# Optimization experiments

Hardware: AMD Instinct MI355X
Metric: run time of the kernel (lower is better)

Reference implementation:

```python
import jax, jax.numpy as jnp
import numpy as np

DIM = 2048
N_HEADS = 16
N_KV_HEADS = 8
HEAD_DIM = DIM // N_HEADS  # 128
N_REP = N_HEADS // N_KV_HEADS
BATCH = 2
SEQ = 2048
CHUNK = 128  # chunked-parallel causal linear attention; SEQ % CHUNK == 0


def _make_freqs_cis(seq_len, head_dim, theta=10000.0):
    freqs = 1.0 / (theta ** (np.arange(0, head_dim, 2, dtype=np.float32) / head_dim))
    t = np.arange(seq_len, dtype=np.float32)
    ang = np.outer(t, freqs)  # [S, D/2]
    return jnp.asarray(np.stack([np.cos(ang), np.sin(ang)], axis=-1))  # [S, D/2, 2]


def setup_inputs() -> dict:
    key = jax.random.key(0)
    ks = jax.random.split(key, 5)
    x = jax.random.normal(ks[0], (BATCH, SEQ, DIM), dtype=jnp.float32)
    freqs_cis = _make_freqs_cis(SEQ, HEAD_DIM)
    s = 0.02
    wq = s * jax.random.normal(ks[1], (N_HEADS * HEAD_DIM, DIM), dtype=jnp.float32)
    wk = s * jax.random.normal(ks[2], (N_KV_HEADS * HEAD_DIM, DIM), dtype=jnp.float32)
    wv = s * jax.random.normal(ks[3], (N_KV_HEADS * HEAD_DIM, DIM), dtype=jnp.float32)
    wo = s * jax.random.normal(ks[4], (DIM, N_HEADS * HEAD_DIM), dtype=jnp.float32)
    return {"x": x, "freqs_cis": freqs_cis, "wq": wq, "wk": wk, "wv": wv, "wo": wo}


def _apply_rotary(x, freqs_cis):
    # x: [B, S, H, D]; freqs_cis: [S, D/2, 2] (cos, sin). Llama pairing: (x0,x1),(x2,x3),...
    B, S, H, D = x.shape
    xr = x.reshape(B, S, H, D // 2, 2)
    x0, x1 = xr[..., 0], xr[..., 1]
    c = freqs_cis[None, :, None, :, 0]
    s = freqs_cis[None, :, None, :, 1]
    o0 = x0 * c - x1 * s
    o1 = x0 * s + x1 * c
    return jnp.stack([o0, o1], axis=-1).reshape(B, S, H, D)


def _causal_linear_attention(q, k, v):
    # q, k, v: [B, H, S, D]; output_i = q_i @ sum_{j<=i} k_j^T v_j
    B, H, S, D = q.shape
    q = jax.nn.softmax(q * (D ** -0.5), axis=-1)  # softmax over feature dim
    k = jax.nn.softmax(k, axis=2)                 # softmax over sequence dim (as in source)
    Nc = S // CHUNK
    qc = q.reshape(B, H, Nc, CHUNK, D)
    kc = k.reshape(B, H, Nc, CHUNK, D)
    vc = v.reshape(B, H, Nc, CHUNK, D)
    # per-chunk KV outer-product sums: [B, H, Nc, D, D]
    kv = jnp.einsum('bhncd,bhnce->bhnde', kc, vc)
    cum = jnp.cumsum(kv, axis=2)
    cum_excl = jnp.concatenate([jnp.zeros_like(cum[:, :, :1]), cum[:, :, :-1]], axis=2)
    inter = jnp.einsum('bhncd,bhnde->bhnce', qc, cum_excl)
    scores = jnp.einsum('bhncd,bhnmd->bhncm', qc, kc)  # [B,H,Nc,C,C]
    mask = jnp.tril(jnp.ones((CHUNK, CHUNK), dtype=bool))
    scores = jnp.where(mask, scores, jnp.zeros((), dtype=scores.dtype))
    intra = jnp.einsum('bhncm,bhnme->bhnce', scores, vc)
    return (inter + intra).reshape(B, H, S, D)


def reference(x, freqs_cis, wq, wk, wv, wo):
    B, S, _ = x.shape
    xq = (x @ wq.T).reshape(B, S, N_HEADS, HEAD_DIM)
    xk = (x @ wk.T).reshape(B, S, N_KV_HEADS, HEAD_DIM)
    xv = (x @ wv.T).reshape(B, S, N_KV_HEADS, HEAD_DIM)
    xq = _apply_rotary(xq, freqs_cis)
    xk = _apply_rotary(xk, freqs_cis)
    # repeat_kv: each kv head repeated N_REP consecutive times
    keys = jnp.repeat(xk, N_REP, axis=2)
    values = jnp.repeat(xv, N_REP, axis=2)
    q = jnp.transpose(xq, (0, 2, 1, 3))
    k = jnp.transpose(keys, (0, 2, 1, 3))
    v = jnp.transpose(values, (0, 2, 1, 3))
    out = _causal_linear_attention(q, k, v)  # [B, H, S, D]
    out = jnp.transpose(out, (0, 2, 1, 3)).reshape(B, S, N_HEADS * HEAD_DIM)
    return out @ wo.T
```

## Files before the change

kernel.cpp:

```cpp
#include <hip/hip_runtime.h>
#include <math.h>

#define DIMV 2048
#define NHEAD 16
#define NKV 8
#define HD 128
#define BATCH 2
#define SEQ 2048
#define CHUNK 128
#define NCHUNK 16
#define MTOK 4096
#define KVD (NKV * HD)

typedef _Float16 half8_t __attribute__((ext_vector_type(8)));
typedef _Float16 half4_t __attribute__((ext_vector_type(4)));
typedef _Float16 half2_t __attribute__((ext_vector_type(2)));
typedef float f32x4 __attribute__((ext_vector_type(4)));

#define GLOBAL_AS __attribute__((address_space(1)))
#define LDS_AS __attribute__((address_space(3)))

#define BARX() __builtin_amdgcn_s_barrier()
#define WAITL(n) asm volatile("s_waitcnt lgkmcnt(" #n ")" ::: "memory")
#define WAITVM(n) asm volatile("s_waitcnt vmcnt(" #n ")" ::: "memory")

__global__ __launch_bounds__(256) void cast_all(const float* __restrict__ x,
                                                const float* __restrict__ wq,
                                                const float* __restrict__ wk,
                                                const float* __restrict__ wv,
                                                const float* __restrict__ wo,
                                                _Float16* __restrict__ xh,
                                                _Float16* __restrict__ wqkvh,
                                                _Float16* __restrict__ woh,
                                                const float* __restrict__ fc,
                                                float* __restrict__ fcT) {
  __shared__ float T[64][65];
  if (blockIdx.x >= 10240) {
    int q = blockIdx.x - 10240;
    int s0 = (q & 31) * 64, d0 = (q >> 5) * 64;
    int t = threadIdx.x;
    int r = t >> 4, c4 = (t & 15) * 4;
#pragma unroll
    for (int p = 0; p < 4; ++p) {
      int sr = p * 16 + r;
      float4 v = *(const float4*)&fc[(size_t)(s0 + sr) * 128 + d0 + c4];
      T[sr][c4] = v.x; T[sr][c4 + 1] = v.y; T[sr][c4 + 2] = v.z; T[sr][c4 + 3] = v.w;
    }
    __syncthreads();
#pragma unroll
    for (int p = 0; p < 4; ++p) {
      int dr = p * 16 + r;
      float4 v = make_float4(T[c4][dr], T[c4 + 1][dr], T[c4 + 2][dr], T[c4 + 3][dr]);
      *(float4*)&fcT[(size_t)(d0 + dr) * SEQ + s0 + c4] = v;
    }
    return;
  }
  long i = (long)(blockIdx.x * 256 + threadIdx.x) * 8;
  const float* src;
  _Float16* dst;
  long off;
  if (i < 8388608)        { src = x;  dst = xh;              off = 0; }
  else if (i < 12582912)  { src = wq; dst = wqkvh;           off = 8388608; }
  else if (i < 14680064)  { src = wk; dst = wqkvh + 4194304; off = 12582912; }
  else if (i < 16777216)  { src = wv; dst = wqkvh + 6291456; off = 14680064; }
  else                    { src = wo; dst = woh;             off = 16777216; }
  long e = i - off;
  float4 a = *(const float4*)&src[e];
  float4 b = *(const float4*)&src[e + 4];
  half8_t h = {(_Float16)a.x, (_Float16)a.y, (_Float16)a.z, (_Float16)a.w,
               (_Float16)b.x, (_Float16)b.y, (_Float16)b.z, (_Float16)b.w};
  *(half8_t*)&dst[e] = h;
}

#define STG_A(bb, kk, i, k0)                                                      \
  __builtin_amdgcn_global_load_lds(                                               \
      (const GLOBAL_AS void*)(A + aoff + (size_t)(i) * 128 * 2048 + (k0) + (kk) * 32), \
      (LDS_AS void*)(As + ((bb) * 2 + (kk)) * 8192 + (i) * 4096 + wave * 512), 16, 0, 0)
#define STG_B(bb, kk, i, k0)                                                      \
  __builtin_amdgcn_global_load_lds(                                               \
      (const GLOBAL_AS void*)(B + boff + (size_t)(i) * 128 * 2048 + (k0) + (kk) * 32), \
      (LDS_AS void*)(Bs + ((bb) * 2 + (kk)) * 8192 + (i) * 4096 + wave * 512), 16, 0, 0)

#define LDA_F(bb, kk, ih) do {                                                    \
    const _Float16* pA_ = As + ((bb) * 2 + (kk)) * 8192 +                         \
                          (wr * 128 + (ih) * 64 + m16) * 32 + pseg8;              \
    af[0] = *(const half8_t*)(pA_);                                               \
    af[1] = *(const half8_t*)(pA_ + 512);                                         \
    af[2] = *(const half8_t*)(pA_ + 1024);                                        \
    af[3] = *(const half8_t*)(pA_ + 1536);                                        \
  } while (0)
#define LDB_F(bb, kk) do {                                                        \
    const _Float16* pB_ = Bs + ((bb) * 2 + (kk)) * 8192 +                         \
                          (wc * 64 + m16) * 32 + pseg8;                           \
    bf[0] = *(const half8_t*)(pB_);                                               \
    bf[1] = *(const half8_t*)(pB_ + 512);                                         \
    bf[2] = *(const half8_t*)(pB_ + 1024);                                        \
    bf[3] = *(const half8_t*)(pB_ + 1536);                                        \
  } while (0)

#define MMX(ih) do {                                                              \
    _Pragma("unroll")                                                             \
    for (int i_ = 0; i_ < 4; ++i_)                                                \
      _Pragma("unroll")                                                           \
      for (int j_ = 0; j_ < 4; ++j_)                                              \
        acc[(ih) * 4 + i_][j_] = __builtin_amdgcn_mfma_f32_16x16x32_f16(          \
            af[i_], bf[j_], acc[(ih) * 4 + i_][j_], 0, 0, 0);                     \
  } while (0)

#define KTILE(bb, k0, DS1, DS2, DS3, DS4, VA, VB) do {                            \
  half8_t af[4], bf[4];                                                           \
  LDA_F(bb, 0, 0); LDB_F(bb, 0);                                                  \
  if (DS1) { STG_A(1 - (bb), 1, 0, (k0) + 64); STG_A(1 - (bb), 1, 1, (k0) + 64); } \
  BARX(); WAITL(0);                                                               \
  __builtin_amdgcn_s_setprio(1); MMX(0); __builtin_amdgcn_s_setprio(0);           \
  BARX();                                                                         \
  LDA_F(bb, 0, 1);                                                                \
  if (DS2) { STG_B(1 - (bb), 1, 0, (k0) + 64); STG_B(1 - (bb), 1, 1, (k0) + 64); } \
  WAITVM(VA);                                                                     \
  BARX(); WAITL(0);                                                               \
  __builtin_amdgcn_s_setprio(1); MMX(1); __builtin_amdgcn_s_setprio(0);           \
  BARX();                                                                         \
  LDA_F(bb, 1, 0); LDB_F(bb, 1);                                                  \
  if (DS3) { STG_A(bb, 0, 0, (k0) + 128); STG_A(bb, 0, 1, (k0) + 128); }          \
  BARX(); WAITL(0);                                                               \
  __builtin_amdgcn_s_setprio(1); MMX(0); __builtin_amdgcn_s_setprio(0);           \
  BARX();                                                                         \
  LDA_F(bb, 1, 1);                                                                \
  if (DS4) { STG_B(bb, 0, 0, (k0) + 128); STG_B(bb, 0, 1, (k0) + 128); }          \
  WAITVM(VB);                                                                     \
  BARX(); WAITL(0);                                                               \
  __builtin_amdgcn_s_setprio(1); MMX(1); __builtin_amdgcn_s_setprio(0);           \
  BARX();                                                                         \
} while (0)

__global__ __launch_bounds__(512, 2) void hgemm_qkv_8p(const _Float16* __restrict__ A,
                                                       const _Float16* __restrict__ B,
                                                       const float* __restrict__ fc,
                                                       _Float16* __restrict__ qh,
                                                       _Float16* __restrict__ kT,
                                                       _Float16* __restrict__ vT) {
  const int K = 2048;
  __shared__ _Float16 As[32768];
  __shared__ _Float16 Bs[32768];
  __shared__ float qsum[4][256];

  const int tid = threadIdx.x;
  const int lane = tid & 63;
  const int wave = tid >> 6;
  const int wr = wave >> 2;
  const int wc = wave & 3;
  const int m16 = lane & 15, quad = lane >> 4;
  const int row0 = blockIdx.y * 256, col0 = blockIdx.x * 256;
  const int pseg8 = (quad ^ ((m16 >> 1) & 3)) * 8;

  const int r_ld = tid >> 2;
  const int sseg = (tid & 3) ^ ((tid >> 3) & 3);
  const size_t aoff = (size_t)(row0 + r_ld) * K + sseg * 8;
  const size_t boff = (size_t)(col0 + r_ld) * K + sseg * 8;

  f32x4 acc[8][4];
#pragma unroll
  for (int m = 0; m < 8; ++m)
#pragma unroll
    for (int j = 0; j < 4; ++j) acc[m][j] = (f32x4){0.f, 0.f, 0.f, 0.f};

  STG_A(0, 0, 0, 0); STG_A(0, 0, 1, 0); STG_B(0, 0, 0, 0); STG_B(0, 0, 1, 0);
  STG_A(0, 1, 0, 0); STG_A(0, 1, 1, 0); STG_B(0, 1, 0, 0); STG_B(0, 1, 1, 0);
  STG_A(1, 0, 0, 64); STG_A(1, 0, 1, 64); STG_B(1, 0, 0, 64); STG_B(1, 0, 1, 64);
  WAITVM(8);
  BARX();

  for (int t = 0; t < 30; t += 2) {
    KTILE(0, t * 64,      1, 1, 1, 1, 8, 8);
    KTILE(1, t * 64 + 64, 1, 1, 1, 1, 8, 8);
  }
  KTILE(0, 1920, 1, 1, 0, 0, 8, 4);
  KTILE(1, 1984, 0, 0, 0, 0, 0, 0);

  if (col0 < 2048) {
    const float sc = 0.08838834764831845f;
    float psum[8][4];
#pragma unroll
    for (int m = 0; m < 8; ++m)
#pragma unroll
      for (int r = 0; r < 4; ++r) psum[m][r] = 0.f;
#pragma unroll
    for (int m = 0; m < 8; ++m)
#pragma unroll
      for (int j = 0; j < 4; ++j) {
        int dl2 = (wc * 64 + j * 16 + m16) & 126;
#pragma unroll
        for (int r = 0; r < 4; ++r) {
          float val = acc[m][j][r];
          float par = __shfl_xor(val, 1);
          int row_l = wr * 128 + (m >> 2) * 64 + (m & 3) * 16 + quad * 4 + r;
          int s_tok = (row0 + row_l) & (SEQ - 1);
          float2 cs = *(const float2*)&fc[(size_t)s_tok * 128 + dl2];
          float o = val * cs.x + par * ((m16 & 1) ? cs.y : -cs.y);
          float e = __expf(o * sc);
          acc[m][j][r] = e;
          psum[m][r] += e;
        }
      }
#pragma unroll
    for (int mm = 1; mm < 16; mm <<= 1)
#pragma unroll
      for (int m = 0; m < 8; ++m)
#pragma unroll
        for (int r = 0; r < 4; ++r) psum[m][r] += __shfl_xor(psum[m][r], mm);
    if (m16 == 0) {
#pragma unroll
      for (int m = 0; m < 8; ++m)
#pragma unroll
        for (int r = 0; r < 4; ++r) {
          int row_l = wr * 128 + (m >> 2) * 64 + (m & 3) * 16 + quad * 4 + r;
          qsum[wc][row_l] = psum[m][r];
        }
    }
    __syncthreads();
#pragma unroll
    for (int m = 0; m < 8; ++m)
#pragma unroll
      for (int r = 0; r < 4; ++r) {
        int row_l = wr * 128 + (m >> 2) * 64 + (m & 3) * 16 + quad * 4 + r;
        psum[m][r] = 1.f / (qsum[wc & 2][row_l] + qsum[(wc & 2) | 1][row_l]);
      }
#pragma unroll
    for (int m = 0; m < 8; ++m)
#pragma unroll
      for (int j = 0; j < 4; ++j) {
        int col = col0 + wc * 64 + j * 16 + m16;
#pragma unroll
        for (int r = 0; r < 4; ++r) {
          int row_l = wr * 128 + (m >> 2) * 64 + (m & 3) * 16 + quad * 4 + r;
          qh[(size_t)(row0 + row_l) * DIMV + col] = (_Float16)(acc[m][j][r] * psum[m][r]);
        }
      }
  } else {
#pragma unroll
    for (int m = 0; m < 8; ++m)
#pragma unroll
      for (int j = 0; j < 4; ++j) {
        int col = col0 + wc * 64 + j * 16 + m16;
        int rowb = row0 + wr * 128 + (m >> 2) * 64 + (m & 3) * 16 + quad * 4;
        half4_t hv = {(_Float16)acc[m][j][0], (_Float16)acc[m][j][1],
                      (_Float16)acc[m][j][2], (_Float16)acc[m][j][3]};
        if (col0 < 3072) {
          *(half4_t*)&kT[(size_t)(col - 2048) * MTOK + rowb] = hv;
        } else {
          *(half4_t*)&vT[(size_t)(col - 3072) * MTOK + rowb] = hv;
        }
      }
  }
}

#define STGBT(bb, kk, k0) do {                                                    \
  __builtin_amdgcn_global_load_lds(                                               \
      (const GLOBAL_AS void*)(A + abase + (k0) + (kk) * 32),                      \
      (LDS_AS void*)(As + ((bb) * 2 + (kk)) * 4096 + wave * 512), 16, 0, 0);      \
  __builtin_amdgcn_global_load_lds(                                               \
      (const GLOBAL_AS void*)(B + bbase + (k0) + (kk) * 32),                      \
      (LDS_AS void*)(Bs + ((bb) * 2 + (kk)) * 8192 + wave * 512), 16, 0, 0);      \
  __builtin_amdgcn_global_load_lds(                                               \
      (const GLOBAL_AS void*)(B + bbase + (size_t)128 * 2048 + (k0) + (kk) * 32), \
      (LDS_AS void*)(Bs + ((bb) * 2 + (kk)) * 8192 + 4096 + wave * 512), 16, 0, 0);\
} while (0)

#define PHASE_BT(bb, kk, SEN, sbb, skk, sk0, VM) do {                             \
  WAITVM(VM);                                                                     \
  BARX();                                                                         \
  half8_t af[4], bf[4];                                                           \
  const _Float16* pA_ = As + ((bb) * 2 + (kk)) * 4096 +                           \
                        (wr * 64 + m16) * 32 + pseg8;                             \
  const _Float16* pB_ = Bs + ((bb) * 2 + (kk)) * 8192 +                           \
                        (wc * 64 + m16) * 32 + pseg8;                             \
  af[0] = *(const half8_t*)(pA_);        af[1] = *(const half8_t*)(pA_ + 512);    \
  af[2] = *(const half8_t*)(pA_ + 1024); af[3] = *(const half8_t*)(pA_ + 1536);   \
  bf[0] = *(const half8_t*)(pB_);        bf[1] = *(const half8_t*)(pB_ + 512);    \
  bf[2] = *(const half8_t*)(pB_ + 1024); bf[3] = *(const half8_t*)(pB_ + 1536);   \
  if (SEN) STGBT(sbb, skk, sk0);                                                  \
  WAITL(0);                                                                       \
  __builtin_amdgcn_s_setprio(1);                                                  \
  _Pragma("unroll")                                                               \
  for (int i_ = 0; i_ < 4; ++i_)                                                  \
    _Pragma("unroll")                                                             \
    for (int j_ = 0; j_ < 4; ++j_)                                                \
      acc[i_][j_] = __builtin_amdgcn_mfma_f32_16x16x32_f16(                       \
          af[i_], bf[j_], acc[i_][j_], 0, 0, 0);                                  \
  __builtin_amdgcn_s_setprio(0);                                                  \
} while (0)

__global__ __launch_bounds__(512, 2) void hgemm_bt_8p(const _Float16* __restrict__ A,
                                                      const _Float16* __restrict__ B,
                                                      float* __restrict__ C) {
  const int K = 2048, N = 2048;
  __shared__ _Float16 As[16384];
  __shared__ _Float16 Bs[32768];

  const int tid = threadIdx.x;
  const int lane = tid & 63;
  const int wave = tid >> 6;
  const int wr = wave >> 2;
  const int wc = wave & 3;
  const int m16 = lane & 15, quad = lane >> 4;
  const int row0 = blockIdx.y * 128, col0 = blockIdx.x * 256;
  const int pseg8 = (quad ^ ((m16 >> 1) & 3)) * 8;

  const int r_ld = tid >> 2;
  const int sseg = (tid & 3) ^ ((tid >> 3) & 3);
  const size_t abase = (size_t)(row0 + r_ld) * K + sseg * 8;
  const size_t bbase = (size_t)(col0 + r_ld) * K + sseg * 8;

  f32x4 acc[4][4];
#pragma unroll
  for (int i = 0; i < 4; ++i)
#pragma unroll
    for (int j = 0; j < 4; ++j) acc[i][j] = (f32x4){0.f, 0.f, 0.f, 0.f};

  STGBT(0, 0, 0); STGBT(0, 1, 0); STGBT(1, 0, 64);

  for (int t = 0; t < 30; ++t) {
    const int bb = t & 1;
    const int k0 = t * 64;
    PHASE_BT(bb, 0, 1, bb ^ 1, 1, k0 + 64, 6);
    PHASE_BT(bb, 1, 1, bb, 0, k0 + 128, 6);
  }
  PHASE_BT(0, 0, 1, 1, 1, 1984, 6);
  PHASE_BT(0, 1, 0, 0, 0, 0, 6);
  PHASE_BT(1, 0, 0, 0, 0, 0, 3);
  PHASE_BT(1, 1, 0, 0, 0, 0, 0);

#pragma unroll
  for (int i = 0; i < 4; ++i)
#pragma unroll
    for (int j = 0; j < 4; ++j) {
      int col = col0 + wc * 64 + j * 16 + m16;
      int rowb = row0 + wr * 64 + i * 16 + quad * 4;
#pragma unroll
      for (int r = 0; r < 4; ++r) C[(size_t)(rowb + r) * N + col] = acc[i][j][r];
    }
}

__global__ __launch_bounds__(256) void k_rope_softmax_T(_Float16* __restrict__ kT,
                                                        const float* __restrict__ fcT) {
  int bi = blockIdx.x;
  int b = bi & 1, pr = bi >> 1;
  int d0 = pr * 2, dl = d0 & 127;
  int t = threadIdx.x;
  size_t r0 = (size_t)d0 * MTOK + b * SEQ + t * 8;
  size_t r1 = r0 + MTOK;
  half8_t x0v = *(half8_t*)&kT[r0];
  half8_t x1v = *(half8_t*)&kT[r1];
  int s8 = t * 8;
  float4 ca = *(const float4*)&fcT[(size_t)dl * SEQ + s8];
  float4 cb = *(const float4*)&fcT[(size_t)dl * SEQ + s8 + 4];
  float4 sa = *(const float4*)&fcT[(size_t)(dl + 1) * SEQ + s8];
  float4 sb = *(const float4*)&fcT[(size_t)(dl + 1) * SEQ + s8 + 4];
  float cc[8] = {ca.x, ca.y, ca.z, ca.w, cb.x, cb.y, cb.z, cb.w};
  float ss[8] = {sa.x, sa.y, sa.z, sa.w, sb.x, sb.y, sb.z, sb.w};
  float e0[8], e1[8];
  float sum0 = 0.f, sum1 = 0.f;
#pragma unroll
  for (int j = 0; j < 8; ++j) {
    float x0 = (float)x0v[j], x1 = (float)x1v[j];
    float o0 = x0 * cc[j] - x1 * ss[j];
    float o1 = x0 * ss[j] + x1 * cc[j];
    e0[j] = expf(o0); e1[j] = expf(o1);
    sum0 += e0[j]; sum1 += e1[j];
  }
#pragma unroll
  for (int off = 1; off < 64; off <<= 1) {
    sum0 += __shfl_xor(sum0, off);
    sum1 += __shfl_xor(sum1, off);
  }
  __shared__ float red[8];
  if ((t & 63) == 0) { red[(t >> 6) * 2] = sum0; red[(t >> 6) * 2 + 1] = sum1; }
  __syncthreads();
  float S0 = red[0] + red[2] + red[4] + red[6];
  float S1 = red[1] + red[3] + red[5] + red[7];
  float i0 = 1.f / S0, i1 = 1.f / S1;
  half8_t w0, w1;
#pragma unroll
  for (int j = 0; j < 8; ++j) {
    w0[j] = (_Float16)(e0[j] * i0);
    w1[j] = (_Float16)(e1[j] * i1);
  }
  *(half8_t*)&kT[r0] = w0;
  *(half8_t*)&kT[r1] = w1;
}

__global__ __launch_bounds__(256) void transpose_k(const _Float16* __restrict__ kT,
                                                   _Float16* __restrict__ kh) {
  __shared__ _Float16 T[64][65];
  int t0 = blockIdx.x * 64, d0 = blockIdx.y * 64;
  int t = threadIdx.x;
  int r = t >> 3, c8 = (t & 7) * 8;
#pragma unroll
  for (int p = 0; p < 2; ++p) {
    int dr = p * 32 + r;
    half8_t v = *(const half8_t*)&kT[(size_t)(d0 + dr) * MTOK + t0 + c8];
#pragma unroll
    for (int j = 0; j < 8; ++j) T[c8 + j][dr] = v[j];
  }
  __syncthreads();
#pragma unroll
  for (int p = 0; p < 2; ++p) {
    int tr = p * 32 + r;
    half8_t v;
#pragma unroll
    for (int j = 0; j < 8; ++j) v[j] = T[tr][c8 + j];
    *(half8_t*)&kh[(size_t)(t0 + tr) * KVD + d0 + c8] = v;
  }
}

__global__ __launch_bounds__(256) void kv_chunk_mfma(const _Float16* __restrict__ vT,
                                                     const _Float16* __restrict__ kT,
                                                     float* __restrict__ kvT) {
  __shared__ _Float16 As[2][128 * 32];
  __shared__ _Float16 Bs[2][128 * 32];
  int bi = blockIdx.x;
  int n = bi & 15, kvh = (bi >> 4) & 7, b = bi >> 7;
  int tok0 = b * SEQ + n * CHUNK;
  const int tid = threadIdx.x;
  const int lane = tid & 63;
  const int wave = tid >> 6;
  const int wr = wave & 1, wc = wave >> 1;
  const int m16 = lane & 15, quad = lane >> 4;
  const int qsw8 = (quad ^ ((m16 >> 1) & 3)) * 8;

  f32x4 acc[4][4];
#pragma unroll
  for (int i = 0; i < 4; ++i)
#pragma unroll
    for (int j = 0; j < 4; ++j) acc[i][j] = (f32x4){0.f, 0.f, 0.f, 0.f};

  const int r_ld = tid >> 2;
  const int sseg = (tid & 3) ^ ((tid >> 3) & 3);
  const size_t a_base = (size_t)(kvh * HD + r_ld) * MTOK + tok0 + sseg * 8;

#pragma unroll
  for (int i = 0; i < 2; ++i) {
    __builtin_amdgcn_global_load_lds(
        (const GLOBAL_AS void*)(vT + a_base + (size_t)i * 64 * MTOK),
        (LDS_AS void*)(&As[0][0] + i * 2048 + wave * 512), 16, 0, 0);
    __builtin_amdgcn_global_load_lds(
        (const GLOBAL_AS void*)(kT + a_base + (size_t)i * 64 * MTOK),
        (LDS_AS void*)(&Bs[0][0] + i * 2048 + wave * 512), 16, 0, 0);
  }

#pragma unroll
  for (int s = 0; s < 4; ++s) {
    WAITVM(0);
    BARX();
    if (s < 3) {
      const int k0 = (s + 1) * 32;
      const int bb = (s + 1) & 1;
#pragma unroll
      for (int i = 0; i < 2; ++i) {
        __builtin_amdgcn_global_load_lds(
            (const GLOBAL_AS void*)(vT + a_base + (size_t)i * 64 * MTOK + k0),
            (LDS_AS void*)(&As[bb][0] + i * 2048 + wave * 512), 16, 0, 0);
        __builtin_amdgcn_global_load_lds(
            (const GLOBAL_AS void*)(kT + a_base + (size_t)i * 64 * MTOK + k0),
            (LDS_AS void*)(&Bs[bb][0] + i * 2048 + wave * 512), 16, 0, 0);
      }
    }
    const _Float16* ra = &As[s & 1][0];
    const _Float16* rb = &Bs[s & 1][0];
    half8_t af[4], bf[4];
#pragma unroll
    for (int i = 0; i < 4; ++i) {
      af[i] = *(const half8_t*)&ra[(wr * 64 + i * 16 + m16) * 32 + qsw8];
      bf[i] = *(const half8_t*)&rb[(wc * 64 + i * 16 + m16) * 32 + qsw8];
    }
#pragma unroll
    for (int i = 0; i < 4; ++i)
#pragma unroll
      for (int j = 0; j < 4; ++j)
        acc[i][j] = __builtin_amdgcn_mfma_f32_16x16x32_f16(af[i], bf[j], acc[i][j], 0, 0, 0);
  }
#pragma unroll
  for (int i = 0; i < 4; ++i)
#pragma unroll
    for (int j = 0; j < 4; ++j) {
      int col = wc * 64 + j * 16 + m16;
      int rowb = wr * 64 + i * 16 + quad * 4;
#pragma unroll
      for (int r = 0; r < 4; ++r)
        kvT[(size_t)bi * 16384 + (size_t)(rowb + r) * 128 + col] = acc[i][j][r];
    }
}

__global__ __launch_bounds__(256) void cumsum_h(const float* __restrict__ kvT,
                                                _Float16* __restrict__ cumh) {
  int gid = blockIdx.x * 256 + threadIdx.x;
  int bk = gid >> 14, idx = gid & 16383;
  size_t base = (size_t)bk * NCHUNK * 16384 + idx;
  float run = 0.f;
#pragma unroll
  for (int n = 0; n < NCHUNK; ++n) {
    cumh[base + (size_t)n * 16384] = (_Float16)run;
    run += kvT[base + (size_t)n * 16384];
  }
}

__global__ __launch_bounds__(256) void attn_fused(const _Float16* __restrict__ qh,
                                                  const _Float16* __restrict__ kh,
                                                  const _Float16* __restrict__ cumh,
                                                  const _Float16* __restrict__ vT,
                                                  _Float16* __restrict__ ath) {
  __shared__ _Float16 QS[128 * 128];
  __shared__ _Float16 Bk[2][128 * 32];
  __shared__ _Float16 Bc[2][128 * 32];
  int bi = blockIdx.x;
  int n = bi & 15, h = (bi >> 4) & 15, b = bi >> 8;
  int kvh = h >> 1;
  int tok0 = b * SEQ + n * CHUNK;
  const int tid = threadIdx.x;
  const int lane = tid & 63;
  const int wave = tid >> 6;
  const int wr = wave & 1, wc = wave >> 1;
  const int m16 = lane & 15, quad = lane >> 4;
  const int qsw8 = (quad ^ ((m16 >> 1) & 3)) * 8;
  const int r_ld = tid >> 2;
  const int sseg = (tid & 3) ^ ((tid >> 3) & 3);

  f32x4 acc[4][4];
  f32x4 accs[4][4];
#pragma unroll
  for (int i = 0; i < 4; ++i)
#pragma unroll
    for (int j = 0; j < 4; ++j) {
      acc[i][j] = (f32x4){0.f, 0.f, 0.f, 0.f};
      accs[i][j] = (f32x4){0.f, 0.f, 0.f, 0.f};
    }

  const int qrow = tid >> 4;
  const int qsl = (tid & 15) ^ (qrow & 7);
  const size_t qsrc = (size_t)(tok0 + qrow) * DIMV + h * HD + qsl * 8;
#pragma unroll
  for (int p = 0; p < 8; ++p)
    __builtin_amdgcn_global_load_lds(
        (const GLOBAL_AS void*)(qh + qsrc + (size_t)p * 16 * DIMV),
        (LDS_AS void*)(QS + p * 2048 + wave * 512), 16, 0, 0);

  const size_t kbase = (size_t)(tok0 + r_ld) * KVD + kvh * HD + sseg * 8;
  const size_t cbase = ((size_t)((b * 8 + kvh) * 16 + n)) * 16384 + (size_t)r_ld * 128 + sseg * 8;
  const size_t vbase = (size_t)(kvh * HD + r_ld) * MTOK + tok0 + sseg * 8;

#pragma unroll
  for (int i = 0; i < 2; ++i) {
    __builtin_amdgcn_global_load_lds(
        (const GLOBAL_AS void*)(kh + kbase + (size_t)i * 64 * KVD),
        (LDS_AS void*)(&Bk[0][0] + i * 2048 + wave * 512), 16, 0, 0);
    __builtin_amdgcn_global_load_lds(
        (const GLOBAL_AS void*)(cumh + cbase + (size_t)i * 64 * 128),
        (LDS_AS void*)(&Bc[0][0] + i * 2048 + wave * 512), 16, 0, 0);
  }

#pragma unroll
  for (int s = 0; s < 8; ++s) {
    WAITVM(0);
    BARX();
    if (s < 3) {
      const int k0 = (s + 1) * 32;
      const int bb = (s + 1) & 1;
#pragma unroll
      for (int i = 0; i < 2; ++i) {
        __builtin_amdgcn_global_load_lds(
            (const GLOBAL_AS void*)(kh + kbase + (size_t)i * 64 * KVD + k0),
            (LDS_AS void*)(&Bk[bb][0] + i * 2048 + wave * 512), 16, 0, 0);
        __builtin_amdgcn_global_load_lds(
            (const GLOBAL_AS void*)(cumh + cbase + (size_t)i * 64 * 128 + k0),
            (LDS_AS void*)(&Bc[bb][0] + i * 2048 + wave * 512), 16, 0, 0);
      }
    } else if (s < 7) {
      const int k0 = (s - 3) * 32;
      const int bb = (s + 1) & 1;
#pragma unroll
      for (int i = 0; i < 2; ++i)
        __builtin_amdgcn_global_load_lds(
            (const GLOBAL_AS void*)(vT + vbase + (size_t)i * 64 * MTOK + k0),
            (LDS_AS void*)(&Bk[bb][0] + i * 2048 + wave * 512), 16, 0, 0);
    }
    if (s < 4) {
      half8_t af[4], bfk[4], bfc[4];
      const int sl4 = s * 4;
      const _Float16* rk = &Bk[s & 1][0];
      const _Float16* rc = &Bc[s & 1][0];
#pragma unroll
      for (int i = 0; i < 4; ++i) {
        int row = wr * 64 + i * 16 + m16;
        af[i] = *(const half8_t*)&QS[row * 128 + ((sl4 + quad) ^ (m16 & 7)) * 8];
        bfk[i] = *(const half8_t*)&rk[(wc * 64 + i * 16 + m16) * 32 + qsw8];
        bfc[i] = *(const half8_t*)&rc[(wc * 64 + i * 16 + m16) * 32 + qsw8];
      }
#pragma unroll
      for (int i = 0; i < 4; ++i)
#pragma unroll
        for (int j = 0; j < 4; ++j) {
          accs[i][j] = __builtin_amdgcn_mfma_f32_16x16x32_f16(af[i], bfk[j], accs[i][j], 0, 0, 0);
          acc[i][j] = __builtin_amdgcn_mfma_f32_16x16x32_f16(af[i], bfc[j], acc[i][j], 0, 0, 0);
        }
      if (s == 3) {
        BARX();
#pragma unroll
        for (int i = 0; i < 4; ++i)
#pragma unroll
          for (int j = 0; j < 4; ++j) {
            int col = wc * 64 + j * 16 + m16;
            int rowb = wr * 64 + i * 16 + quad * 4;
#pragma unroll
            for (int r = 0; r < 4; ++r) {
              int row = rowb + r;
              float v = (col <= row) ? accs[i][j][r] : 0.f;
              int sp = (col >> 3) ^ (row & 7);
              QS[row * 128 + sp * 8 + (col & 7)] = (_Float16)v;
            }
          }
        WAITL(0);
      }
    } else {
      half8_t af[4], bf[4];
      const int sl4 = (s - 4) * 4;
      const _Float16* rk = &Bk[s & 1][0];
#pragma unroll
      for (int i = 0; i < 4; ++i) {
        int row = wr * 64 + i * 16 + m16;
        af[i] = *(const half8_t*)&QS[row * 128 + ((sl4 + quad) ^ (m16 & 7)) * 8];
        bf[i] = *(const half8_t*)&rk[(wc * 64 + i * 16 + m16) * 32 + qsw8];
      }
#pragma unroll
      for (int i = 0; i < 4; ++i)
#pragma unroll
        for (int j = 0; j < 4; ++j)
          acc[i][j] = __builtin_amdgcn_mfma_f32_16x16x32_f16(af[i], bf[j], acc[i][j], 0, 0, 0);
    }
  }

#pragma unroll
  for (int i = 0; i < 4; ++i)
#pragma unroll
    for (int j = 0; j < 4; ++j) {
      int col = wc * 64 + j * 16 + m16;
      int rowb = wr * 64 + i * 16 + quad * 4;
#pragma unroll
      for (int r = 0; r < 4; ++r)
        ath[(size_t)(tok0 + rowb + r) * DIMV + h * HD + col] = (_Float16)acc[i][j][r];
    }
}

extern "C" void kernel_launch(void* const* d_in, const int* in_sizes, int n_in,
                              void* d_out, int out_size, void* d_ws, size_t ws_size,
                              hipStream_t stream) {
  const float* x  = (const float*)d_in[0];
  const float* fc = (const float*)d_in[1];
  const float* wq = (const float*)d_in[2];
  const float* wk = (const float*)d_in[3];
  const float* wv = (const float*)d_in[4];
  const float* wo = (const float*)d_in[5];
  float* out = (float*)d_out;

  char* p = (char*)d_ws;
  _Float16* xh    = (_Float16*)p;  p += 16777216;
  _Float16* wqkvh = (_Float16*)p;  p += 16777216;
  _Float16* woh   = (_Float16*)p;  p += 8388608;
  _Float16* qh    = (_Float16*)p;  p += 16777216;
  _Float16* kT    = (_Float16*)p;  p += 8388608;
  _Float16* kh    = (_Float16*)p;  p += 8388608;
  _Float16* vT    = (_Float16*)p;  p += 8388608;
  float*    kvT   = (float*)p;     p += 16777216;
  _Float16* cumh  = (_Float16*)p;  p += 8388608;
  _Float16* ath   = (_Float16*)p;  p += 16777216;
  float*    fcT   = (float*)p;     p += 1048576;

  cast_all<<<10304, 256, 0, stream>>>(x, wq, wk, wv, wo, xh, wqkvh, woh, fc, fcT);

  hgemm_qkv_8p<<<dim3(16, 16), 512, 0, stream>>>(xh, wqkvh, fc, qh, kT, vT);

  k_rope_softmax_T<<<1024, 256, 0, stream>>>(kT, fcT);
  transpose_k<<<dim3(64, 16), 256, 0, stream>>>(kT, kh);

  kv_chunk_mfma<<<256, 256, 0, stream>>>(vT, kT, kvT);
  cumsum_h<<<1024, 256, 0, stream>>>(kvT, cumh);

  attn_fused<<<512, 256, 0, stream>>>(qh, kh, cumh, vT, ath);

  hgemm_bt_8p<<<dim3(8, 32), 512, 0, stream>>>(ath, woh, out);
}
```

Measured before the change: 285.3 us.

## Restructure QKV GEMM k-loop into full-tile phases with fewer barriers

Replaces the four half-tile MFMA phases per k-tile in the QKV projection GEMM with two phases. Each phase loads all 8 A fragments and 4 B fragments and issues 32 MFMAs, and the A and B global-to-LDS stages for a future sub-tile are issued together. This halves the number of barrier and LDS-wait points per k-step, reducing sync overhead. It costs more live registers (8 A fragments), coarser overlap between loads and compute, and a changed row mapping in the epilogue.

```diff
diff --git a/kernel.cpp b/kernel.cpp
--- a/kernel.cpp
+++ b/kernel.cpp
@@ -81,55 +81,30 @@
       (const GLOBAL_AS void*)(B + boff + (size_t)(i) * 128 * 2048 + (k0) + (kk) * 32), \
       (LDS_AS void*)(Bs + ((bb) * 2 + (kk)) * 8192 + (i) * 4096 + wave * 512), 16, 0, 0)
 
-#define LDA_F(bb, kk, ih) do {                                                    \
-    const _Float16* pA_ = As + ((bb) * 2 + (kk)) * 8192 +                         \
-                          (wr * 128 + (ih) * 64 + m16) * 32 + pseg8;              \
-    af[0] = *(const half8_t*)(pA_);                                               \
-    af[1] = *(const half8_t*)(pA_ + 512);                                         \
-    af[2] = *(const half8_t*)(pA_ + 1024);                                        \
-    af[3] = *(const half8_t*)(pA_ + 1536);                                        \
-  } while (0)
-#define LDB_F(bb, kk) do {                                                        \
-    const _Float16* pB_ = Bs + ((bb) * 2 + (kk)) * 8192 +                         \
-                          (wc * 64 + m16) * 32 + pseg8;                           \
-    bf[0] = *(const half8_t*)(pB_);                                               \
-    bf[1] = *(const half8_t*)(pB_ + 512);                                         \
-    bf[2] = *(const half8_t*)(pB_ + 1024);                                        \
-    bf[3] = *(const half8_t*)(pB_ + 1536);                                        \
-  } while (0)
-
-#define MMX(ih) do {                                                              \
+#define KT2(bb, kk, SEN, sbb, skk, sk0, VM) do {                                  \
+  half8_t af[8], bf[4];                                                           \
+  const _Float16* pA_ = As + ((bb) * 2 + (kk)) * 8192 +                           \
+                        (wr * 128 + m16) * 32 + pseg8;                            \
+  const _Float16* pB_ = Bs + ((bb) * 2 + (kk)) * 8192 +                           \
+                        (wc * 64 + m16) * 32 + pseg8;                             \
+  _Pragma("unroll")                                                               \
+  for (int m_ = 0; m_ < 8; ++m_) af[m_] = *(const half8_t*)(pA_ + m_ * 512);      \
+  _Pragma("unroll")                                                               \
+  for (int j_ = 0; j_ < 4; ++j_) bf[j_] = *(const half8_t*)(pB_ + j_ * 512);      \
+  if (SEN) {                                                                      \
+    STG_A(sbb, skk, 0, sk0); STG_A(sbb, skk, 1, sk0);                             \
+    STG_B(sbb, skk, 0, sk0); STG_B(sbb, skk, 1, sk0);                             \
+  }                                                                               \
+  WAITVM(VM);                                                                     \
+  BARX(); WAITL(0);                                                               \
+  __builtin_amdgcn_s_setprio(1);                                                  \
+  _Pragma("unroll")                                                               \
+  for (int m_ = 0; m_ < 8; ++m_)                                                  \
     _Pragma("unroll")                                                             \
-    for (int i_ = 0; i_ < 4; ++i_)                                                \
-      _Pragma("unroll")                                                           \
-      for (int j_ = 0; j_ < 4; ++j_)                                              \
-        acc[(ih) * 4 + i_][j_] = __builtin_amdgcn_mfma_f32_16x16x32_f16(          \
-            af[i_], bf[j_], acc[(ih) * 4 + i_][j_], 0, 0, 0);                     \
-  } while (0)
-
-#define KTILE(bb, k0, DS1, DS2, DS3, DS4, VA, VB) do {                            \
-  half8_t af[4], bf[4];                                                           \
-  LDA_F(bb, 0, 0); LDB_F(bb, 0);                                                  \
-  if (DS1) { STG_A(1 - (bb), 1, 0, (k0) + 64); STG_A(1 - (bb), 1, 1, (k0) + 64); } \
-  BARX(); WAITL(0);                                                               \
-  __builtin_amdgcn_s_setprio(1); MMX(0); __builtin_amdgcn_s_setprio(0);           \
-  BARX();                                                                         \
-  LDA_F(bb, 0, 1);                                                                \
-  if (DS2) { STG_B(1 - (bb), 1, 0, (k0) + 64); STG_B(1 - (bb), 1, 1, (k0) + 64); } \
-  WAITVM(VA);                                                                     \
-  BARX(); WAITL(0);                                                               \
-  __builtin_amdgcn_s_setprio(1); MMX(1); __builtin_amdgcn_s_setprio(0);           \
-  BARX();                                                                         \
-  LDA_F(bb, 1, 0); LDB_F(bb, 1);                                                  \
-  if (DS3) { STG_A(bb, 0, 0, (k0) + 128); STG_A(bb, 0, 1, (k0) + 128); }          \
-  BARX(); WAITL(0);                                                               \
-  __builtin_amdgcn_s_setprio(1); MMX(0); __builtin_amdgcn_s_setprio(0);           \
-  BARX();                                                                         \
-  LDA_F(bb, 1, 1);                                                                \
-  if (DS4) { STG_B(bb, 0, 0, (k0) + 128); STG_B(bb, 0, 1, (k0) + 128); }          \
-  WAITVM(VB);                                                                     \
-  BARX(); WAITL(0);                                                               \
-  __builtin_amdgcn_s_setprio(1); MMX(1); __builtin_amdgcn_s_setprio(0);           \
+    for (int j_ = 0; j_ < 4; ++j_)                                                \
+      acc[m_][j_] = __builtin_amdgcn_mfma_f32_16x16x32_f16(                       \
+          af[m_], bf[j_], acc[m_][j_], 0, 0, 0);                                  \
+  __builtin_amdgcn_s_setprio(0);                                                  \
   BARX();                                                                         \
 } while (0)
 
@@ -170,12 +145,16 @@
   WAITVM(8);
   BARX();
 
-  for (int t = 0; t < 30; t += 2) {
-    KTILE(0, t * 64,      1, 1, 1, 1, 8, 8);
-    KTILE(1, t * 64 + 64, 1, 1, 1, 1, 8, 8);
-  }
-  KTILE(0, 1920, 1, 1, 0, 0, 8, 4);
-  KTILE(1, 1984, 0, 0, 0, 0, 0, 0);
+  for (int t = 0; t < 30; ++t) {
+    const int bb = t & 1;
+    const int k0 = t * 64;
+    KT2(bb, 0, 1, bb ^ 1, 1, k0 + 64, 8);
+    KT2(bb, 1, 1, bb, 0, k0 + 128, 8);
+  }
+  KT2(0, 0, 1, 1, 1, 1984, 8);
+  KT2(0, 1, 0, 0, 0, 0, 4);
+  KT2(1, 0, 0, 0, 0, 0, 0);
+  KT2(1, 1, 0, 0, 0, 0, 0);
 
   if (col0 < 2048) {
     const float sc = 0.08838834764831845f;
@@ -193,7 +172,7 @@
         for (int r = 0; r < 4; ++r) {
           float val = acc[m][j][r];
           float par = __shfl_xor(val, 1);
-          int row_l = wr * 128 + (m >> 2) * 64 + (m & 3) * 16 + quad * 4 + r;
+          int row_l = wr * 128 + m * 16 + quad * 4 + r;
           int s_tok = (row0 + row_l) & (SEQ - 1);
           float2 cs = *(const float2*)&fc[(size_t)s_tok * 128 + dl2];
           float o = val * cs.x + par * ((m16 & 1) ? cs.y : -cs.y);
@@ -213,7 +192,7 @@
       for (int m = 0; m < 8; ++m)
 #pragma unroll
         for (int r = 0; r < 4; ++r) {
-          int row_l = wr * 128 + (m >> 2) * 64 + (m & 3) * 16 + quad * 4 + r;
+          int row_l = wr * 128 + m * 16 + quad * 4 + r;
           qsum[wc][row_l] = psum[m][r];
         }
     }
@@ -222,7 +201,7 @@
     for (int m = 0; m < 8; ++m)
 #pragma unroll
       for (int r = 0; r < 4; ++r) {
-        int row_l = wr * 128 + (m >> 2) * 64 + (m & 3) * 16 + quad * 4 + r;
+        int row_l = wr * 128 + m * 16 + quad * 4 + r;
         psum[m][r] = 1.f / (qsum[wc & 2][row_l] + qsum[(wc & 2) | 1][row_l]);
       }
 #pragma unroll
@@ -232,7 +211,7 @@
         int col = col0 + wc * 64 + j * 16 + m16;
 #pragma unroll
         for (int r = 0; r < 4; ++r) {
-          int row_l = wr * 128 + (m >> 2) * 64 + (m & 3) * 16 + quad * 4 + r;
+          int row_l = wr * 128 + m * 16 + quad * 4 + r;
           qh[(size_t)(row0 + row_l) * DIMV + col] = (_Float16)(acc[m][j][r] * psum[m][r]);
         }
       }
@@ -242,7 +221,7 @@
 #pragma unroll
       for (int j = 0; j < 4; ++j) {
         int col = col0 + wc * 64 + j * 16 + m16;
-        int rowb = row0 + wr * 128 + (m >> 2) * 64 + (m & 3) * 16 + quad * 4;
+        int rowb = row0 + wr * 128 + m * 16 + quad * 4;
         half4_t hv = {(_Float16)acc[m][j][0], (_Float16)acc[m][j][1],
                       (_Float16)acc[m][j][2], (_Float16)acc[m][j][3]};
         if (col0 < 3072) {
```

New measurement: 282.0 us, median of 2. No clear change (-1.2%).
